# Kernel optimization log

Measured on AMD Instinct MI355X. Metric: run time of the kernel, lower is better.

## Reference

```python
import jax, jax.numpy as jnp
import numpy as np
from jax import lax

IH, IW = 32, 32
N = IH * IW
C = 256
HEADS = 8
DH = C // HEADS
SCALE = 32 ** -0.5  # uses dim_head arg (32), as in the torch module
EPS = 1e-6


def _rel_index():
    coords = np.stack(np.meshgrid(np.arange(IH), np.arange(IW), indexing='ij')).reshape(2, -1)
    rel = coords[:, :, None] - coords[:, None, :]  # [2, n, n]
    rel[0] += IH - 1
    rel[1] += IW - 1
    rel[0] *= 2 * IW - 1
    return jnp.asarray(rel.sum(0).reshape(-1))  # [n*n] int

REL_IDX = _rel_index()


def _conv3(x, W):
    # 3x3 conv, stride 1, pad 1, no bias; NCHW / OIHW
    return lax.conv_general_dilated(x, W, (1, 1), 'SAME',
                                    dimension_numbers=('NCHW', 'OIHW', 'NCHW'))


def _proj(x, W, g, b):
    # conv3x3 -> GroupNorm(1 group, per-channel affine) -> exact GELU -> split heads
    y = _conv3(x, W)
    m = jnp.mean(y, axis=(1, 2, 3), keepdims=True)
    v = jnp.var(y, axis=(1, 2, 3), keepdims=True)
    y = (y - m) * lax.rsqrt(v + EPS) * g[None, :, None, None] + b[None, :, None, None]
    y = jax.nn.gelu(y, approximate=False)
    B = y.shape[0]
    # b c h w -> b (h d heads split) : channel c = head*DH + d  -> b h n d
    return y.reshape(B, HEADS, DH, N).transpose(0, 1, 3, 2)


def setup_inputs() -> dict:
    key = jax.random.key(0)
    ks = jax.random.split(key, 8)
    s = 0.02
    return {
        'x': jax.random.normal(ks[0], (8, C, IH, IW), dtype=jnp.float32),
        'Wq': jax.random.normal(ks[1], (C, C, 3, 3), dtype=jnp.float32) * s,
        'gq': jnp.ones((C,), jnp.float32), 'bq': jnp.zeros((C,), jnp.float32),
        'Wk': jax.random.normal(ks[2], (C, C, 3, 3), dtype=jnp.float32) * s,
        'gk': jnp.ones((C,), jnp.float32), 'bk': jnp.zeros((C,), jnp.float32),
        'Wv': jax.random.normal(ks[3], (C, C, 3, 3), dtype=jnp.float32) * s,
        'gv': jnp.ones((C,), jnp.float32), 'bv': jnp.zeros((C,), jnp.float32),
        'bias_table': jax.random.normal(ks[4], ((2 * IH - 1) * (2 * IW - 1), HEADS), dtype=jnp.float32) * s,
        'Wout': jax.random.normal(ks[5], (C, C, 1, 1), dtype=jnp.float32) * s,
        'bout': jnp.zeros((C,), jnp.float32),
    }


def reference(x, Wq, gq, bq, Wk, gk, bk, Wv, gv, bv, bias_table, Wout, bout):
    B = x.shape[0]
    q = _proj(x, Wq, gq, bq)  # [B, H, N, DH]
    k = _proj(x, Wk, gk, bk)
    v = _proj(x, Wv, gv, bv)
    dots = jnp.einsum('bhnd,bhmd->bhnm', q, k) * SCALE  # [B, H, N, N]
    # gather relative position bias: [n*n, heads] -> [1, heads, n, n]
    bias = bias_table[REL_IDX].reshape(N, N, HEADS).transpose(2, 0, 1)[None]
    attn = jax.nn.softmax(dots + bias, axis=-1)
    out = jnp.einsum('bhnm,bhmd->bhnd', attn, v)  # [B, H, N, DH]
    # b h n d -> b n (h d) -> b c ih iw
    out = out.transpose(0, 2, 1, 3).reshape(B, N, C).transpose(0, 2, 1).reshape(B, C, IH, IW)
    # 1x1 conv projection with bias (Dropout2d is identity at eval)
    out = jnp.einsum('oc,bchw->bohw', Wout[:, :, 0, 0], out) + bout[None, :, None, None]
    return out
```

## Files before the change

### kernel.cpp

```cpp
#include <hip/hip_runtime.h>

typedef float f32x4 __attribute__((ext_vector_type(4)));
typedef short bf16x8 __attribute__((ext_vector_type(8)));
typedef short bf16x4 __attribute__((ext_vector_type(4)));

#define PADN 1156

typedef const __attribute__((address_space(1))) void* gptr_t;
typedef __attribute__((address_space(3))) void* lptr_t;

__device__ __forceinline__ short f2b(float f) {
  unsigned u = __float_as_uint(f);
  unsigned r = (u + 0x7FFFu + ((u >> 16) & 1u)) >> 16;
  return (short)r;
}
__device__ __forceinline__ float b2f(short s) {
  return __uint_as_float(((unsigned)(unsigned short)s) << 16);
}

__global__ __launch_bounds__(256) void prep_x(const float* __restrict__ x,
                                              short* __restrict__ xpad) {
  __shared__ float tile[32][33];
  int wg = blockIdx.x;
  int b = wg >> 8, rem = wg & 255;
  int cb = rem >> 5, sb = rem & 31;
  int t = threadIdx.x;
  int sl = t & 31, cq = t >> 5;
  const float* xb = x + ((b * 256 + cb * 32) * 1024) + sb * 32;
#pragma unroll
  for (int i = 0; i < 4; i++) {
    int cl = cq + i * 8;
    tile[cl][sl] = xb[cl * 1024 + sl];
  }
  __syncthreads();
  int cl2 = t & 31, sq = t >> 5;
  short* xp = xpad + b * (PADN * 256) + cb * 32 + cl2;
#pragma unroll
  for (int i = 0; i < 4; i++) {
    int sl2 = sq + i * 8;
    int s = sb * 32 + sl2;
    int pidx = ((s >> 5) + 1) * 34 + (s & 31) + 1;
    xp[pidx * 256] = f2b(tile[cl2][sl2]);
  }
}

__global__ __launch_bounds__(256) void prep_w(const float* __restrict__ Wq,
                                              const float* __restrict__ Wk,
                                              const float* __restrict__ Wv,
                                              const float* __restrict__ Wout,
                                              short* __restrict__ wpack,
                                              short* __restrict__ woutp) {
  int blk = blockIdx.x;
  int tid = threadIdx.x;
  if (blk < 768) {
    __shared__ float lds[2304];
    int p = blk >> 8, o = blk & 255;
    const float* W = (p == 0) ? Wq : (p == 1) ? Wk : Wv;
    const float* src = W + o * 2304;
    for (int i = tid; i < 2304; i += 256) lds[i] = src[i];
    __syncthreads();
    short* dst = wpack + p * 589824 + o * 2304;
#pragma unroll
    for (int t = 0; t < 9; t++) dst[t * 256 + tid] = f2b(lds[tid * 9 + t]);
  } else {
    int e = (blk - 768) * 1024 + tid * 4;
    f32x4 v = *(const f32x4*)(Wout + e);
    bf16x4 o4;
#pragma unroll
    for (int j = 0; j < 4; j++) o4[j] = f2b(v[j]);
    *(bf16x4*)(woutp + e) = o4;
  }
}

__global__ __launch_bounds__(256) void bias_mat(const float* __restrict__ btab,
                                                short* __restrict__ biasP) {
  int id = blockIdx.x * 256 + threadIdx.x;
  int lane = id & 63;
  int rest = id >> 6;
  int jt = rest & 3; rest >>= 2;
  int kb = rest & 15; rest >>= 4;
  int qblk = rest & 63; rest >>= 6;
  int h = rest;
  int li = lane & 15, g = lane >> 4;
  int qrow = qblk * 16 + li;
  int yi = qrow >> 5, xi = qrow & 31;
  int ibase = (yi + 31) * 63 + (xi + 31);
  int j0 = kb * 64 + jt * 16 + g * 4;
  int yj = j0 >> 5, xj0 = j0 & 31;
  int idx0 = ibase - yj * 63 - xj0;
  const float L2E = 1.4426950408889634f;
  bf16x4 v;
#pragma unroll
  for (int rr = 0; rr < 4; rr++) v[rr] = f2b(btab[(idx0 - rr) * 8 + h] * L2E);
  *(bf16x4*)(biasP + (size_t)id * 4) = v;
}

__global__ __launch_bounds__(256, 2) void conv_gemm(const short* __restrict__ xpad,
                                                    const short* __restrict__ wpack,
                                                    short* __restrict__ qn,
                                                    short* __restrict__ kn,
                                                    short* __restrict__ vn,
                                                    float* __restrict__ stats) {
  __shared__ short ldsA[2][8192];
  __shared__ short ldsB[2][8192];
  int wg = blockIdx.x;
  int b = wg / 48;
  int rr0 = wg - b * 48;
  int p = (rr0 < 16) ? 0 : (rr0 < 32) ? 1 : 2;
  int t16 = rr0 & 15;
  bool xA = (p < 2);
  int mt_i = xA ? (t16 >> 1) : (t16 >> 3);
  int nt_i = xA ? (t16 & 1) : (t16 & 7);
  int m0 = mt_i * 128, n0 = nt_i * 128;
  int tid = threadIdx.x;
  int lane = tid & 63, wave = tid >> 6;
  int wr = wave >> 1, wc = wave & 1;
  int g = lane >> 4, li = lane & 15;

  const char* xb = (const char*)(xpad + b * (PADN * 256));
  const char* wp = (const char*)(wpack + p * (256 * 2304));
  const char* abase = xA ? xb : wp;
  const char* bbase = xA ? wp : xb;

  int srow = tid >> 3;
  int schunk = ((tid & 7) ^ (srow & 7)) * 16;
  int aoff[4], boff[4];
#pragma unroll
  for (int q = 0; q < 4; q++) {
    int row = m0 + q * 32 + srow;
    aoff[q] = (xA ? ((((row >> 5) + 1) * 34 + (row & 31) + 1) * 512) : (row * 4608)) + schunk;
  }
#pragma unroll
  for (int q = 0; q < 4; q++) {
    int row = n0 + q * 32 + srow;
    boff[q] = (xA ? (row * 4608) : ((((row >> 5) + 1) * 34 + (row & 31) + 1) * 512)) + schunk;
  }

  int aadr[4][2], badr[4][2];
#pragma unroll
  for (int mt = 0; mt < 4; mt++) {
    int row = wr * 64 + mt * 16 + li;
#pragma unroll
    for (int ksub = 0; ksub < 2; ksub++)
      aadr[mt][ksub] = row * 64 + (((ksub * 4 + g) ^ (row & 7)) * 8);
  }
#pragma unroll
  for (int nt = 0; nt < 4; nt++) {
    int row = wc * 64 + nt * 16 + li;
#pragma unroll
    for (int ksub = 0; ksub < 2; ksub++)
      badr[nt][ksub] = row * 64 + (((ksub * 4 + g) ^ (row & 7)) * 8);
  }

#define STAGE(KS, BUF) do {                                                        \
    int t_ = (KS) >> 2, cq_ = (KS) & 3;                                            \
    int ty_ = (t_ * 11) >> 5;                                                      \
    int doff_ = (ty_ - 1) * 34 + (t_ - 3 * ty_) - 1;                               \
    int kA_ = (xA ? doff_ * 512 : t_ * 512) + cq_ * 128;                           \
    int kB_ = (xA ? t_ * 512 : doff_ * 512) + cq_ * 128;                           \
    _Pragma("unroll")                                                              \
    for (int q_ = 0; q_ < 4; q_++)                                                 \
      __builtin_amdgcn_global_load_lds((gptr_t)(abase + aoff[q_] + kA_),           \
                                       (lptr_t)&ldsA[BUF][(q_ * 256 + tid) * 8],   \
                                       16, 0, 0);                                  \
    _Pragma("unroll")                                                              \
    for (int q_ = 0; q_ < 4; q_++)                                                 \
      __builtin_amdgcn_global_load_lds((gptr_t)(bbase + boff[q_] + kB_),           \
                                       (lptr_t)&ldsB[BUF][(q_ * 256 + tid) * 8],   \
                                       16, 0, 0);                                  \
  } while (0)

  f32x4 acc[4][4] = {};
  STAGE(0, 0);
  __syncthreads();
#pragma unroll 2
  for (int ks = 0; ks < 36; ks++) {
    int cur = ks & 1;
    if (ks < 35) STAGE(ks + 1, cur ^ 1);
    bf16x8 af[4][2], bfv[4][2];
#pragma unroll
    for (int mt = 0; mt < 4; mt++)
#pragma unroll
      for (int ksub = 0; ksub < 2; ksub++)
        af[mt][ksub] = *(const bf16x8*)&ldsA[cur][aadr[mt][ksub]];
#pragma unroll
    for (int nt = 0; nt < 4; nt++)
#pragma unroll
      for (int ksub = 0; ksub < 2; ksub++)
        bfv[nt][ksub] = *(const bf16x8*)&ldsB[cur][badr[nt][ksub]];
#pragma unroll
    for (int ksub = 0; ksub < 2; ksub++)
#pragma unroll
      for (int mt = 0; mt < 4; mt++)
#pragma unroll
        for (int nt = 0; nt < 4; nt++)
          acc[mt][nt] = __builtin_amdgcn_mfma_f32_16x16x32_bf16(af[mt][ksub], bfv[nt][ksub], acc[mt][nt], 0, 0, 0);
    __syncthreads();
  }
#undef STAGE

  short* outp = (p == 0) ? qn : (p == 1) ? kn : vn;
  int ostride = xA ? 256 : 1024;
  int obase = b * 262144;
  float s1 = 0.f, s2 = 0.f;
#pragma unroll
  for (int mt = 0; mt < 4; mt++)
#pragma unroll
    for (int nt = 0; nt < 4; nt++) {
      int col = n0 + wc * 64 + nt * 16 + li;
#pragma unroll
      for (int rr = 0; rr < 4; rr++) {
        int row = m0 + wr * 64 + mt * 16 + g * 4 + rr;
        float v = acc[mt][nt][rr];
        s1 += v;
        s2 += v * v;
        outp[obase + row * ostride + col] = f2b(v);
      }
    }
#pragma unroll
  for (int off = 1; off < 64; off <<= 1) {
    s1 += __shfl_xor(s1, off);
    s2 += __shfl_xor(s2, off);
  }
  if (lane == 0) {
    atomicAdd(&stats[(b * 3 + p) * 2], s1);
    atomicAdd(&stats[(b * 3 + p) * 2 + 1], s2);
  }
}

__global__ __launch_bounds__(256) void norm_gelu(const short* __restrict__ qn, const short* __restrict__ kn,
                                                 const short* __restrict__ vn,
                                                 short* __restrict__ qpk, short* __restrict__ kpk,
                                                 short* __restrict__ vpk,
                                                 const float* __restrict__ stats,
                                                 const float* __restrict__ gq, const float* __restrict__ bq,
                                                 const float* __restrict__ gk, const float* __restrict__ bk,
                                                 const float* __restrict__ gv, const float* __restrict__ bv) {
  long e = ((long)blockIdx.x * 256 + threadIdx.x) * 8;
  int buf = (int)(e >> 21);
  int w = (int)(e & 2097151);
  int b = w >> 18;
  int pos = w & 262143;
  const short* base = (buf == 0) ? qn : (buf == 1) ? kn : vn;
  const float* gg = (buf == 0) ? gq : (buf == 1) ? gk : gv;
  const float* bb = (buf == 0) ? bq : (buf == 1) ? bk : bv;
  float s1 = stats[(b * 3 + buf) * 2];
  float s2 = stats[(b * 3 + buf) * 2 + 1];
  float mean = s1 * (1.f / 262144.f);
  float var = s2 * (1.f / 262144.f) - mean * mean;
  float rstd = rsqrtf(var + 1e-6f);
  const float PS = 0.17677669529663687f * 1.4426950408889634f;
  float post = (buf == 0) ? PS : 1.f;
  bf16x8 v = *(const bf16x8*)(base + (size_t)b * 262144 + pos);
#pragma unroll
  for (int j = 0; j < 8; j++) {
    int ch = (buf < 2) ? ((pos + j) & 255) : ((pos + j) >> 10);
    float y = b2f(v[j]);
    y = (y - mean) * rstd * gg[ch] + bb[ch];
    y = 0.5f * y * (1.f + erff(y * 0.70710678118f));
    v[j] = f2b(y * post);
  }
  if (buf < 2) {
    int s = pos >> 8, c = pos & 255;
    int h2 = c >> 5, g2 = (c >> 3) & 3;
    short* dst = (buf == 0) ? qpk : kpk;
    size_t addr = ((size_t)((b * 8 + h2) * 64 + (s >> 4))) * 512 + (g2 * 16 + (s & 15)) * 8;
    *(bf16x8*)(dst + addr) = v;
  } else {
    int c = pos >> 10, s0 = pos & 1023;
    int h2 = c >> 5, d = c & 31;
    int dblk = d >> 4, liv = d & 15;
    int kv32 = s0 >> 5, jr0 = s0 & 31;
    int hi = jr0 >> 4, g0 = (jr0 >> 2) & 3;
    size_t addr = ((size_t)((b * 8 + h2) * 32 + kv32) * 2 + dblk) * 512 + hi * 4 + liv * 8;
    bf16x4 lo4 = {v[0], v[1], v[2], v[3]};
    bf16x4 hi4 = {v[4], v[5], v[6], v[7]};
    *(bf16x4*)(vpk + addr + g0 * 128) = lo4;
    *(bf16x4*)(vpk + addr + (g0 + 1) * 128) = hi4;
  }
}

__global__ __launch_bounds__(256, 4) void attn(const short* __restrict__ qpk,
                                               const short* __restrict__ kpk,
                                               const short* __restrict__ vpk,
                                               const short* __restrict__ biasP,
                                               short* __restrict__ obuf) {
  int wg = blockIdx.x;
  int b = wg >> 7, rem = wg & 127;
  int h = rem >> 4, qt = rem & 15;
  int lane = threadIdx.x & 63, wave = threadIdx.x >> 6;
  int g = lane >> 4, li = lane & 15;
  int qblk = qt * 4 + wave;
  int qbase = qblk * 16;
  const short* qpb = qpk + ((size_t)((b * 8 + h) * 64 + qblk)) * 512;
  const short* kpb = kpk + ((size_t)((b * 8 + h) * 64)) * 512;
  const short* vpb = vpk + ((size_t)(b * 8 + h)) * 32768;
  const short* bpb = biasP + (((size_t)(h * 64 + qblk)) << 14) + lane * 4;
  bf16x8 qf = *(const bf16x8*)(qpb + lane * 8);
  float m = -1e30f, l = 0.f;
  f32x4 oacc[2] = {};
  bf16x8 kf[4];
  bf16x4 bfr[4];
#pragma unroll
  for (int jt = 0; jt < 4; jt++) {
    kf[jt] = *(const bf16x8*)(kpb + jt * 512 + lane * 8);
    bfr[jt] = *(const bf16x4*)(bpb + jt * 256);
  }
#pragma unroll 1
  for (int kb = 0; kb < 16; kb++) {
    f32x4 st[4];
#pragma unroll
    for (int jt = 0; jt < 4; jt++) {
      f32x4 cinit;
#pragma unroll
      for (int rr = 0; rr < 4; rr++) cinit[rr] = b2f(bfr[jt][rr]);
      st[jt] = __builtin_amdgcn_mfma_f32_16x16x32_bf16(kf[jt], qf, cinit, 0, 0, 0);
    }
    bf16x8 kf2[4];
    bf16x4 bfr2[4];
    if (kb < 15) {
#pragma unroll
      for (int jt = 0; jt < 4; jt++) {
        kf2[jt] = *(const bf16x8*)(kpb + ((kb + 1) * 4 + jt) * 512 + lane * 8);
        bfr2[jt] = *(const bf16x4*)(bpb + (kb + 1) * 1024 + jt * 256);
      }
    }
    bf16x8 vf[2][2];
#pragma unroll
    for (int nt = 0; nt < 2; nt++)
#pragma unroll
      for (int ks = 0; ks < 2; ks++)
        vf[nt][ks] = *(const bf16x8*)(vpb + ((kb * 2 + ks) * 2 + nt) * 512 + lane * 8);
    float mb = -1e30f;
#pragma unroll
    for (int jt = 0; jt < 4; jt++)
#pragma unroll
      for (int rr = 0; rr < 4; rr++) mb = fmaxf(mb, st[jt][rr]);
    mb = fmaxf(mb, __shfl_xor(mb, 16));
    mb = fmaxf(mb, __shfl_xor(mb, 32));
    if (!__all(mb <= m + 8.f)) {
      float mnew = fmaxf(m, mb);
      float alpha = exp2f(m - mnew);
      m = mnew;
      l *= alpha;
#pragma unroll
      for (int rr = 0; rr < 4; rr++) {
        float ar = __shfl(alpha, (lane & 0x30) | (g * 4 + rr));
        oacc[0][rr] *= ar;
        oacc[1][rr] *= ar;
      }
    }
    float ls = 0.f;
    bf16x8 pf0, pf1;
#pragma unroll
    for (int jt = 0; jt < 4; jt++)
#pragma unroll
      for (int rr = 0; rr < 4; rr++) {
        float pe = exp2f(st[jt][rr] - m);
        ls += pe;
        int q2 = jt * 4 + rr;
        if (q2 < 8) pf0[q2] = f2b(pe); else pf1[q2 - 8] = f2b(pe);
      }
    ls += __shfl_xor(ls, 16);
    ls += __shfl_xor(ls, 32);
    l += ls;
#pragma unroll
    for (int nt = 0; nt < 2; nt++)
#pragma unroll
      for (int ks = 0; ks < 2; ks++)
        oacc[nt] = __builtin_amdgcn_mfma_f32_16x16x32_bf16(ks == 0 ? pf0 : pf1, vf[nt][ks], oacc[nt], 0, 0, 0);
    if (kb < 15) {
#pragma unroll
      for (int jt = 0; jt < 4; jt++) {
        kf[jt] = kf2[jt];
        bfr[jt] = bfr2[jt];
      }
    }
  }
  float linv = 1.f / l;
  short* ob = obuf + (b * 1024) * 256 + h * 32;
#pragma unroll
  for (int rr = 0; rr < 4; rr++) {
    float lr = __shfl(linv, (lane & 0x30) | (g * 4 + rr));
    int row = qbase + g * 4 + rr;
    ob[row * 256 + li] = f2b(oacc[0][rr] * lr);
    ob[row * 256 + 16 + li] = f2b(oacc[1][rr] * lr);
  }
}

__global__ __launch_bounds__(256) void out_gemm(const short* __restrict__ woutp,
                                                const short* __restrict__ obuf,
                                                const float* __restrict__ bout,
                                                float* __restrict__ out) {
  int wg = blockIdx.x;
  int b = wg >> 5, rem = wg & 31;
  int mt_i = rem >> 4, nt_i = rem & 15;
  int m0 = mt_i * 128, n0 = nt_i * 64;
  int lane = threadIdx.x & 63, wave = threadIdx.x >> 6;
  int wr = wave >> 1, wc = wave & 1;
  int g = lane >> 4, li = lane & 15;
  int aoff[4];
#pragma unroll
  for (int mt = 0; mt < 4; mt++) aoff[mt] = (m0 + wr * 64 + mt * 16 + li) * 256;
  int boff[2];
#pragma unroll
  for (int nt = 0; nt < 2; nt++) boff[nt] = (b * 1024 + n0 + wc * 32 + nt * 16 + li) * 256;
  f32x4 acc[4][2] = {};
#pragma unroll
  for (int ks = 0; ks < 8; ks++) {
    int kof = ks * 32 + g * 8;
    bf16x8 af[4], bfr[2];
#pragma unroll
    for (int mt = 0; mt < 4; mt++) af[mt] = *(const bf16x8*)(woutp + aoff[mt] + kof);
#pragma unroll
    for (int nt = 0; nt < 2; nt++) bfr[nt] = *(const bf16x8*)(obuf + boff[nt] + kof);
#pragma unroll
    for (int mt = 0; mt < 4; mt++)
#pragma unroll
      for (int nt = 0; nt < 2; nt++)
        acc[mt][nt] = __builtin_amdgcn_mfma_f32_16x16x32_bf16(af[mt], bfr[nt], acc[mt][nt], 0, 0, 0);
  }
#pragma unroll
  for (int mt = 0; mt < 4; mt++)
#pragma unroll
    for (int nt = 0; nt < 2; nt++) {
      int col = n0 + wc * 32 + nt * 16 + li;
#pragma unroll
      for (int rr = 0; rr < 4; rr++) {
        int row = m0 + wr * 64 + mt * 16 + g * 4 + rr;
        out[b * 262144 + row * 1024 + col] = acc[mt][nt][rr] + bout[row];
      }
    }
}

extern "C" void kernel_launch(void* const* d_in, const int* in_sizes, int n_in,
                              void* d_out, int out_size, void* d_ws, size_t ws_size,
                              hipStream_t stream) {
  const float* x = (const float*)d_in[0];
  const float* Wq = (const float*)d_in[1];
  const float* gq = (const float*)d_in[2];
  const float* bq = (const float*)d_in[3];
  const float* Wk = (const float*)d_in[4];
  const float* gk = (const float*)d_in[5];
  const float* bk = (const float*)d_in[6];
  const float* Wv = (const float*)d_in[7];
  const float* gv = (const float*)d_in[8];
  const float* bv = (const float*)d_in[9];
  const float* btab = (const float*)d_in[10];
  const float* Wout = (const float*)d_in[11];
  const float* bout = (const float*)d_in[12];
  float* out = (float*)d_out;

  char* ws = (char*)d_ws;
  size_t off = 0;
  float* stats = (float*)(ws + off); off += 256;
  short* xpad = (short*)(ws + off); off += (size_t)8 * PADN * 256 * 2;
  short* wpack = (short*)(ws + off); off += (size_t)3 * 256 * 2304 * 2;
  short* woutp = (short*)(ws + off); off += (size_t)256 * 256 * 2;
  short* qn = (short*)(ws + off); off += (size_t)4194304;
  short* kn = (short*)(ws + off); off += (size_t)4194304;
  short* vn = (short*)(ws + off); off += (size_t)4194304;
  short* obuf = (short*)(ws + off); off += (size_t)4194304;
  short* qpk = (short*)(ws + off); off += (size_t)4194304;
  short* kpk = (short*)(ws + off); off += (size_t)4194304;
  short* vpk = (short*)(ws + off); off += (size_t)4194304;
  short* biasP = (short*)(ws + off); off += (size_t)8 * 1024 * 1024 * 2;
  if (ws_size < off) return;

  hipMemsetAsync(stats, 0, 256, stream);
  hipMemsetAsync(xpad, 0, (size_t)8 * PADN * 256 * 2, stream);
  prep_x<<<2048, 256, 0, stream>>>(x, xpad);
  prep_w<<<832, 256, 0, stream>>>(Wq, Wk, Wv, Wout, wpack, woutp);
  bias_mat<<<8192, 256, 0, stream>>>(btab, biasP);
  conv_gemm<<<384, 256, 0, stream>>>(xpad, wpack, qn, kn, vn, stats);
  norm_gelu<<<3072, 256, 0, stream>>>(qn, kn, vn, qpk, kpk, vpk, stats, gq, bq, gk, bk, gv, bv);
  attn<<<1024, 256, 0, stream>>>(qpk, kpk, vpk, biasP, obuf);
  out_gemm<<<256, 256, 0, stream>>>(woutp, obuf, bout, out);
}
```

Before: 160.3 us.

## Merge prep kernels and fold bias-matrix build into conv_gemm tail blocks

The x and weight prep kernels become a single launch, and the relative-position bias matrix is built by 2048 extra blocks appended to the conv GEMM grid, each handling 1024 entries. This drops two kernel launches and lets the bias gather run alongside the GEMM blocks instead of serially. The GEMM block index is also remapped so consecutive blocks cycle across batches, which changes how work is spread over CUs. The bias blocks allocate the GEMM's large LDS footprint and may compete with GEMM tiles for CU slots.

```diff
diff --git a/kernel.cpp b/kernel.cpp
--- a/kernel.cpp
+++ b/kernel.cpp
@@ -18,81 +18,58 @@
   return __uint_as_float(((unsigned)(unsigned short)s) << 16);
 }
 
-__global__ __launch_bounds__(256) void prep_x(const float* __restrict__ x,
-                                              short* __restrict__ xpad) {
-  __shared__ float tile[32][33];
-  int wg = blockIdx.x;
-  int b = wg >> 8, rem = wg & 255;
-  int cb = rem >> 5, sb = rem & 31;
+__global__ __launch_bounds__(256) void prep(const float* __restrict__ x,
+                                            const float* __restrict__ Wq,
+                                            const float* __restrict__ Wk,
+                                            const float* __restrict__ Wv,
+                                            const float* __restrict__ Wout,
+                                            short* __restrict__ xpad,
+                                            short* __restrict__ wpack,
+                                            short* __restrict__ woutp) {
+  __shared__ float lds[2304];
+  int blk0 = blockIdx.x;
   int t = threadIdx.x;
-  int sl = t & 31, cq = t >> 5;
-  const float* xb = x + ((b * 256 + cb * 32) * 1024) + sb * 32;
-#pragma unroll
-  for (int i = 0; i < 4; i++) {
-    int cl = cq + i * 8;
-    tile[cl][sl] = xb[cl * 1024 + sl];
-  }
-  __syncthreads();
-  int cl2 = t & 31, sq = t >> 5;
-  short* xp = xpad + b * (PADN * 256) + cb * 32 + cl2;
-#pragma unroll
-  for (int i = 0; i < 4; i++) {
-    int sl2 = sq + i * 8;
-    int s = sb * 32 + sl2;
-    int pidx = ((s >> 5) + 1) * 34 + (s & 31) + 1;
-    xp[pidx * 256] = f2b(tile[cl2][sl2]);
-  }
-}
-
-__global__ __launch_bounds__(256) void prep_w(const float* __restrict__ Wq,
-                                              const float* __restrict__ Wk,
-                                              const float* __restrict__ Wv,
-                                              const float* __restrict__ Wout,
-                                              short* __restrict__ wpack,
-                                              short* __restrict__ woutp) {
-  int blk = blockIdx.x;
-  int tid = threadIdx.x;
-  if (blk < 768) {
-    __shared__ float lds[2304];
-    int p = blk >> 8, o = blk & 255;
-    const float* W = (p == 0) ? Wq : (p == 1) ? Wk : Wv;
-    const float* src = W + o * 2304;
-    for (int i = tid; i < 2304; i += 256) lds[i] = src[i];
+  if (blk0 < 2048) {
+    int wg = blk0;
+    int b = wg >> 8, rem = wg & 255;
+    int cb = rem >> 5, sb = rem & 31;
+    int sl = t & 31, cq = t >> 5;
+    const float* xb = x + ((b * 256 + cb * 32) * 1024) + sb * 32;
+#pragma unroll
+    for (int i = 0; i < 4; i++) {
+      int cl = cq + i * 8;
+      lds[cl * 33 + sl] = xb[cl * 1024 + sl];
+    }
     __syncthreads();
-    short* dst = wpack + p * 589824 + o * 2304;
-#pragma unroll
-    for (int t = 0; t < 9; t++) dst[t * 256 + tid] = f2b(lds[tid * 9 + t]);
+    int cl2 = t & 31, sq = t >> 5;
+    short* xp = xpad + b * (PADN * 256) + cb * 32 + cl2;
+#pragma unroll
+    for (int i = 0; i < 4; i++) {
+      int sl2 = sq + i * 8;
+      int s = sb * 32 + sl2;
+      int pidx = ((s >> 5) + 1) * 34 + (s & 31) + 1;
+      xp[pidx * 256] = f2b(lds[cl2 * 33 + sl2]);
+    }
   } else {
-    int e = (blk - 768) * 1024 + tid * 4;
-    f32x4 v = *(const f32x4*)(Wout + e);
-    bf16x4 o4;
-#pragma unroll
-    for (int j = 0; j < 4; j++) o4[j] = f2b(v[j]);
-    *(bf16x4*)(woutp + e) = o4;
-  }
-}
-
-__global__ __launch_bounds__(256) void bias_mat(const float* __restrict__ btab,
-                                                short* __restrict__ biasP) {
-  int id = blockIdx.x * 256 + threadIdx.x;
-  int lane = id & 63;
-  int rest = id >> 6;
-  int jt = rest & 3; rest >>= 2;
-  int kb = rest & 15; rest >>= 4;
-  int qblk = rest & 63; rest >>= 6;
-  int h = rest;
-  int li = lane & 15, g = lane >> 4;
-  int qrow = qblk * 16 + li;
-  int yi = qrow >> 5, xi = qrow & 31;
-  int ibase = (yi + 31) * 63 + (xi + 31);
-  int j0 = kb * 64 + jt * 16 + g * 4;
-  int yj = j0 >> 5, xj0 = j0 & 31;
-  int idx0 = ibase - yj * 63 - xj0;
-  const float L2E = 1.4426950408889634f;
-  bf16x4 v;
-#pragma unroll
-  for (int rr = 0; rr < 4; rr++) v[rr] = f2b(btab[(idx0 - rr) * 8 + h] * L2E);
-  *(bf16x4*)(biasP + (size_t)id * 4) = v;
+    int blk = blk0 - 2048;
+    if (blk < 768) {
+      int p = blk >> 8, o = blk & 255;
+      const float* W = (p == 0) ? Wq : (p == 1) ? Wk : Wv;
+      const float* src = W + o * 2304;
+      for (int i = t; i < 2304; i += 256) lds[i] = src[i];
+      __syncthreads();
+      short* dst = wpack + p * 589824 + o * 2304;
+#pragma unroll
+      for (int tt = 0; tt < 9; tt++) dst[tt * 256 + t] = f2b(lds[t * 9 + tt]);
+    } else {
+      int e = (blk - 768) * 1024 + t * 4;
+      f32x4 v = *(const f32x4*)(Wout + e);
+      bf16x4 o4;
+#pragma unroll
+      for (int j = 0; j < 4; j++) o4[j] = f2b(v[j]);
+      *(bf16x4*)(woutp + e) = o4;
+    }
+  }
 }
 
 __global__ __launch_bounds__(256, 2) void conv_gemm(const short* __restrict__ xpad,
@@ -100,10 +77,39 @@
                                                     short* __restrict__ qn,
                                                     short* __restrict__ kn,
                                                     short* __restrict__ vn,
-                                                    float* __restrict__ stats) {
+                                                    float* __restrict__ stats,
+                                                    const float* __restrict__ btab,
+                                                    short* __restrict__ biasP) {
   __shared__ short ldsA[2][8192];
   __shared__ short ldsB[2][8192];
-  int wg = blockIdx.x;
+  int bid = blockIdx.x;
+  int tid = threadIdx.x;
+  if (bid >= 384) {
+    const float L2E = 1.4426950408889634f;
+#pragma unroll
+    for (int it = 0; it < 4; it++) {
+      int id = (bid - 384) * 1024 + it * 256 + tid;
+      int lane = id & 63;
+      int rest = id >> 6;
+      int jt = rest & 3; rest >>= 2;
+      int kb = rest & 15; rest >>= 4;
+      int qblk = rest & 63; rest >>= 6;
+      int h = rest;
+      int li = lane & 15, g = lane >> 4;
+      int qrow = qblk * 16 + li;
+      int yi = qrow >> 5, xi = qrow & 31;
+      int ibase = (yi + 31) * 63 + (xi + 31);
+      int j0 = kb * 64 + jt * 16 + g * 4;
+      int yj = j0 >> 5, xj0 = j0 & 31;
+      int idx0 = ibase - yj * 63 - xj0;
+      bf16x4 v;
+#pragma unroll
+      for (int rr = 0; rr < 4; rr++) v[rr] = f2b(btab[(idx0 - rr) * 8 + h] * L2E);
+      *(bf16x4*)(biasP + (size_t)id * 4) = v;
+    }
+    return;
+  }
+  int wg = (bid & 7) * 48 + (bid >> 3);
   int b = wg / 48;
   int rr0 = wg - b * 48;
   int p = (rr0 < 16) ? 0 : (rr0 < 32) ? 1 : 2;
@@ -112,7 +118,6 @@
   int mt_i = xA ? (t16 >> 1) : (t16 >> 3);
   int nt_i = xA ? (t16 & 1) : (t16 & 7);
   int m0 = mt_i * 128, n0 = nt_i * 128;
-  int tid = threadIdx.x;
   int lane = tid & 63, wave = tid >> 6;
   int wr = wave >> 1, wc = wave & 1;
   int g = lane >> 4, li = lane & 15;
@@ -469,10 +474,8 @@
 
   hipMemsetAsync(stats, 0, 256, stream);
   hipMemsetAsync(xpad, 0, (size_t)8 * PADN * 256 * 2, stream);
-  prep_x<<<2048, 256, 0, stream>>>(x, xpad);
-  prep_w<<<832, 256, 0, stream>>>(Wq, Wk, Wv, Wout, wpack, woutp);
-  bias_mat<<<8192, 256, 0, stream>>>(btab, biasP);
-  conv_gemm<<<384, 256, 0, stream>>>(xpad, wpack, qn, kn, vn, stats);
+  prep<<<2880, 256, 0, stream>>>(x, Wq, Wk, Wv, Wout, xpad, wpack, woutp);
+  conv_gemm<<<2432, 256, 0, stream>>>(xpad, wpack, qn, kn, vn, stats, btab, biasP);
   norm_gelu<<<3072, 256, 0, stream>>>(qn, kn, vn, qpk, kpk, vpk, stats, gq, bq, gk, bk, gv, bv);
   attn<<<1024, 256, 0, stream>>>(qpk, kpk, vpk, biasP, obuf);
   out_gemm<<<256, 256, 0, stream>>>(woutp, obuf, bout, out);
```

After: 141.8 us. 11.6% less time.
